# Performance work log

Measured on AMD Instinct MI355X. Metric: run time of the kernel, lower is better.

Reference implementation:

```python
import jax, jax.numpy as jnp
import numpy as np

EPS = 1e-5
SCALE = 2
K_UP = 5


def _conv(x, w, pad):
    return jax.lax.conv_general_dilated(
        x, w, window_strides=(1, 1), padding=[(pad, pad), (pad, pad)],
        dimension_numbers=("NCHW", "OIHW", "NCHW"))


def _bn(x, gamma, beta, mean, var):
    scale = gamma / jnp.sqrt(var + EPS)
    return x * scale[None, :, None, None] + (beta - mean * scale)[None, :, None, None]


def _pixel_shuffle(x, r):
    b, cr2, h, w = x.shape
    c = cr2 // (r * r)
    x = x.reshape(b, c, r, r, h, w)
    x = x.transpose(0, 1, 4, 2, 5, 3)  # b, c, h, r, w, r
    return x.reshape(b, c, h * r, w * r)


def setup_inputs() -> dict:
    key = jax.random.key(0)
    ks = jax.random.split(key, 6)
    c, c_mid, k_enc = 256, 64, 3
    n_k = (SCALE * K_UP) ** 2  # 100
    return {
        "x": jax.random.normal(ks[0], (2, c, 64, 64), jnp.float32),
        "comp_w": jax.random.normal(ks[1], (c_mid, c, 1, 1), jnp.float32) * 0.05,
        "comp_gamma": jnp.ones((c_mid,), jnp.float32),
        "comp_beta": jnp.zeros((c_mid,), jnp.float32),
        "comp_mean": jax.random.normal(ks[2], (c_mid,), jnp.float32) * 0.1,
        "comp_var": jax.random.uniform(ks[3], (c_mid,), jnp.float32, 0.5, 1.5),
        "enc_w": jax.random.normal(ks[4], (n_k, c_mid, k_enc, k_enc), jnp.float32) * 0.05,
        "enc_gamma": jnp.ones((n_k,), jnp.float32),
        "enc_beta": jnp.zeros((n_k,), jnp.float32),
        "enc_mean": jax.random.normal(ks[5], (n_k,), jnp.float32) * 0.1,
        "enc_var": jnp.ones((n_k,), jnp.float32),
    }


def reference(x, comp_w, comp_gamma, comp_beta, comp_mean, comp_var,
              enc_w, enc_gamma, enc_beta, enc_mean, enc_var):
    b, c, h, w = x.shape
    h_, w_ = h * SCALE, w * SCALE
    # comp: 1x1 conv -> BN -> ReLU
    W = jax.nn.relu(_bn(_conv(x, comp_w, 0), comp_gamma, comp_beta, comp_mean, comp_var))
    # enc: 3x3 conv -> BN (no relu)
    W = _bn(_conv(W, enc_w, 1), enc_gamma, enc_beta, enc_mean, enc_var)
    # pixel shuffle to [b, k_up^2, h_, w_] then softmax over kernel dim
    W = _pixel_shuffle(W, SCALE)
    W = jax.nn.softmax(W, axis=1)
    # nearest upsample x2
    Xu = jnp.repeat(jnp.repeat(x, SCALE, axis=2), SCALE, axis=3)
    # unfold: kernel k_up, dilation=SCALE, padding=k_up//2*SCALE
    pad = (K_UP // 2) * SCALE
    Xp = jnp.pad(Xu, ((0, 0), (0, 0), (pad, pad), (pad, pad)))
    patches = jnp.stack(
        [Xp[:, :, i * SCALE:i * SCALE + h_, j * SCALE:j * SCALE + w_]
         for i in range(K_UP) for j in range(K_UP)], axis=2)  # [b,c,k^2,h_,w_]
    return jnp.einsum("bkhw,bckhw->bchw", W, patches)
```

## Files before the change

kernel.cpp:

```cpp
#include <hip/hip_runtime.h>
#include <hip/hip_bf16.h>

typedef __hip_bfloat16 bf16;
#define EPSF 1e-5f

__global__ void k1_comp(const float* __restrict__ x, const float* __restrict__ w,
                        const float* __restrict__ gamma, const float* __restrict__ beta,
                        const float* __restrict__ mean, const float* __restrict__ var,
                        float* __restrict__ comp) {
    __shared__ float shx[2][32 * 64];
    const int pxt = blockIdx.x;
    const int ocg = blockIdx.y;
    const int b   = blockIdx.z;
    const int tid  = threadIdx.x;
    const int wave = tid >> 6, lane = tid & 63;
    const int oc0 = ocg * 32 + wave * 8;
    const int px0 = pxt << 6;
    const float* xb = x + b * (256 * 4096) + px0;

    float acc[8] = {0.f, 0.f, 0.f, 0.f, 0.f, 0.f, 0.f, 0.f};

    #pragma unroll
    for (int i = 0; i < 2; ++i) {
        int f4  = tid * 2 + i;
        int row = f4 >> 4, col4 = f4 & 15;
        float4 v = *(const float4*)(xb + row * 4096 + col4 * 4);
        *(float4*)(&shx[0][row * 64 + col4 * 4]) = v;
    }
    __syncthreads();

    for (int icc = 0; icc < 8; ++icc) {
        const int buf = icc & 1;
        if (icc < 7) {
            #pragma unroll
            for (int i = 0; i < 2; ++i) {
                int f4  = tid * 2 + i;
                int row = f4 >> 4, col4 = f4 & 15;
                float4 v = *(const float4*)(xb + ((icc + 1) * 32 + row) * 4096 + col4 * 4);
                *(float4*)(&shx[buf ^ 1][row * 64 + col4 * 4]) = v;
            }
        }
        #pragma unroll 8
        for (int ic_l = 0; ic_l < 32; ++ic_l) {
            float xv = shx[buf][ic_l * 64 + lane];
            const float* wp = w + icc * 32 + ic_l;
            #pragma unroll
            for (int m = 0; m < 8; ++m)
                acc[m] += xv * wp[(oc0 + m) * 256];
        }
        __syncthreads();
    }
    #pragma unroll
    for (int m = 0; m < 8; ++m) {
        int mo = oc0 + m;
        float s = gamma[mo] * rsqrtf(var[mo] + EPSF);
        float r = acc[m] * s + (beta[mo] - mean[mo] * s);
        comp[(b * 64 + mo) * 4096 + px0 + lane] = fmaxf(r, 0.f);
    }
}

__global__ void k2_enc_part(const float* __restrict__ comp, const float* __restrict__ w,
                            float* __restrict__ encp) {
    __shared__ float sh[8 * 630];
    const int tile = blockIdx.x;
    const int og   = blockIdx.y >> 2;
    const int icc  = blockIdx.y & 3;
    const int b    = blockIdx.z;
    const int ty0 = (tile >> 1) << 4;
    const int tx0 = (tile & 1) << 5;
    const int tid = threadIdx.x;
    const int tx = tid & 15, ty = tid >> 4;
    const int o0 = og * 5;

    float accA[5], accB[5];
    #pragma unroll
    for (int i = 0; i < 5; ++i) { accA[i] = 0.f; accB[i] = 0.f; }

    for (int ics = 0; ics < 2; ++ics) {
        if (ics) __syncthreads();
        const float* cb = comp + (b * 64 + icc * 16 + ics * 8) * 4096;
        for (int idx = tid; idx < 8 * 612; idx += 256) {
            int ic_l = idx / 612;
            int rem  = idx - ic_l * 612;
            int r = rem / 34;
            int c = rem - r * 34;
            int gy = ty0 + r - 1;
            int gx = tx0 + c - 1;
            float v = 0.f;
            if (gy >= 0 && gy < 64 && gx >= 0 && gx < 64)
                v = cb[(ic_l << 12) + (gy << 6) + gx];
            sh[ic_l * 630 + r * 35 + c] = v;
        }
        __syncthreads();

        #pragma unroll 2
        for (int ic_l = 0; ic_l < 8; ++ic_l) {
            const float* base = sh + ic_l * 630 + ty * 35 + 2 * tx;
            float t[3][4];
            #pragma unroll
            for (int dy = 0; dy < 3; ++dy)
                #pragma unroll
                for (int dx = 0; dx < 4; ++dx)
                    t[dy][dx] = base[dy * 35 + dx];
            const int ic = icc * 16 + ics * 8 + ic_l;
            #pragma unroll
            for (int o_l = 0; o_l < 5; ++o_l) {
                const float* wp = w + ((o0 + o_l) * 64 + ic) * 9;
                #pragma unroll
                for (int dy = 0; dy < 3; ++dy)
                    #pragma unroll
                    for (int dx = 0; dx < 3; ++dx) {
                        float wv = wp[dy * 3 + dx];
                        accA[o_l] += wv * t[dy][dx];
                        accB[o_l] += wv * t[dy][dx + 1];
                    }
            }
        }
    }
    const int pix = ((ty0 + ty) << 6) + tx0 + 2 * tx;
    #pragma unroll
    for (int o_l = 0; o_l < 5; ++o_l) {
        float2 v = {accA[o_l], accB[o_l]};
        *(float2*)(&encp[((icc * 2 + b) * 100 + o0 + o_l) * 4096 + pix]) = v;
    }
}

__global__ void k3_softmax(const float* __restrict__ encp,
                           const float* __restrict__ gamma, const float* __restrict__ beta,
                           const float* __restrict__ mean, const float* __restrict__ var,
                           bf16* __restrict__ Wsm) {
    int t = blockIdx.x * 64 + threadIdx.x;
    int pos = t & 4095;
    int g   = (t >> 12) & 3;
    int b   = t >> 14;
    float v[25];
    float mx = -1e30f;
    #pragma unroll
    for (int k = 0; k < 25; ++k) {
        int o = k * 4 + g;
        float a = 0.f;
        #pragma unroll
        for (int icc = 0; icc < 4; ++icc)
            a += encp[((icc * 2 + b) * 100 + o) * 4096 + pos];
        float s = gamma[o] * rsqrtf(var[o] + EPSF);
        v[k] = a * s + (beta[o] - mean[o] * s);
        mx = fmaxf(mx, v[k]);
    }
    float s = 0.f;
    #pragma unroll
    for (int k = 0; k < 25; ++k) { v[k] = __expf(v[k] - mx); s += v[k]; }
    float inv = 1.f / s;
    bf16* o = Wsm + ((b * 4 + g) * 25) * 4096 + pos;
    #pragma unroll
    for (int k = 0; k < 25; ++k) o[k * 4096] = __float2bfloat16(v[k] * inv);
}

__global__ void k4_gather(const float* __restrict__ x, const bf16* __restrict__ Wsm,
                          float* __restrict__ out) {
    __shared__ float4 patch[12 * 21];
    const int tile   = blockIdx.x;
    const int cchunk = blockIdx.y;
    const int b      = blockIdx.z;
    const int ly0 = (tile >> 2) << 3;
    const int lx0 = (tile & 3) << 4;
    const int tid = threadIdx.x;
    const int ph = tid >> 7;
    const int r  = tid & 127;
    const int ly = r >> 4, lx = r & 15;
    const int yl = ly0 + ly, xl = lx0 + lx;

    float w0[25], w1[25];
    {
        const bf16* wp0 = Wsm + ((b * 4 + ph * 2    ) * 25) * 4096 + yl * 64 + xl;
        const bf16* wp1 = Wsm + ((b * 4 + ph * 2 + 1) * 25) * 4096 + yl * 64 + xl;
        #pragma unroll
        for (int k = 0; k < 25; ++k) {
            w0[k] = __bfloat162float(wp0[k * 4096]);
            w1[k] = __bfloat162float(wp1[k * 4096]);
        }
    }
    const int pr = tid / 20, pc = tid % 20;
    const int gy = ly0 - 2 + pr, gx = lx0 - 2 + pc;
    const bool inb = (tid < 240) && (gy >= 0) && (gy < 64) && (gx >= 0) && (gx < 64);

    for (int cg = 0; cg < 4; ++cg) {
        const int c0 = cchunk * 16 + cg * 4;
        if (tid < 240) {
            float4 v = {0.f, 0.f, 0.f, 0.f};
            if (inb) {
                const float* xp = x + ((b * 256 + c0) * 4096) + gy * 64 + gx;
                v.x = xp[0]; v.y = xp[4096]; v.z = xp[8192]; v.w = xp[12288];
            }
            patch[pr * 21 + pc] = v;
        }
        __syncthreads();
        float4 a0 = {0.f, 0.f, 0.f, 0.f};
        float4 a1 = {0.f, 0.f, 0.f, 0.f};
        #pragma unroll
        for (int i = 0; i < 5; ++i) {
            #pragma unroll
            for (int j = 0; j < 5; ++j) {
                float4 xv = patch[(ly + i) * 21 + (lx + j)];
                float wa = w0[i * 5 + j], wb = w1[i * 5 + j];
                a0.x += wa * xv.x; a0.y += wa * xv.y; a0.z += wa * xv.z; a0.w += wa * xv.w;
                a1.x += wb * xv.x; a1.y += wb * xv.y; a1.z += wb * xv.z; a1.w += wb * xv.w;
            }
        }
        float* ob = out + (b * 256 + c0) * 16384 + (2 * yl + ph) * 128 + 2 * xl;
        float2 s0 = {a0.x, a1.x}; *(float2*)(ob)           = s0;
        float2 s1 = {a0.y, a1.y}; *(float2*)(ob + 16384)   = s1;
        float2 s2 = {a0.z, a1.z}; *(float2*)(ob + 32768)   = s2;
        float2 s3 = {a0.w, a1.w}; *(float2*)(ob + 49152)   = s3;
        __syncthreads();
    }
}

extern "C" void kernel_launch(void* const* d_in, const int* in_sizes, int n_in,
                              void* d_out, int out_size, void* d_ws, size_t ws_size,
                              hipStream_t stream) {
    const float* x          = (const float*)d_in[0];
    const float* comp_w     = (const float*)d_in[1];
    const float* comp_gamma = (const float*)d_in[2];
    const float* comp_beta  = (const float*)d_in[3];
    const float* comp_mean  = (const float*)d_in[4];
    const float* comp_var   = (const float*)d_in[5];
    const float* enc_w      = (const float*)d_in[6];
    const float* enc_gamma  = (const float*)d_in[7];
    const float* enc_beta   = (const float*)d_in[8];
    const float* enc_mean   = (const float*)d_in[9];
    const float* enc_var    = (const float*)d_in[10];
    float* out = (float*)d_out;

    float* ws   = (float*)d_ws;
    float* comp = ws;
    float* encp = ws + 524288;
    bf16*  Wsm  = (bf16*)(ws + 524288 + 3276800);

    k1_comp<<<dim3(64, 2, 2), dim3(256), 0, stream>>>(x, comp_w, comp_gamma, comp_beta,
                                                      comp_mean, comp_var, comp);
    k2_enc_part<<<dim3(8, 80, 2), dim3(256), 0, stream>>>(comp, enc_w, encp);
    k3_softmax<<<dim3(512), dim3(64), 0, stream>>>(encp, enc_gamma, enc_beta,
                                                   enc_mean, enc_var, Wsm);
    k4_gather<<<dim3(32, 16, 2), dim3(256), 0, stream>>>(x, Wsm, out);
}
```

Baseline: 154.9 us.

## Repack softmax weights pixel-major, split softmax across lanes, double-buffer gather patches

The softmax kernel now gives each pixel to four lanes, each handling eight of the 25 kernel taps, and combines the max and sum with cross-lane shuffles. It writes the bf16 weights in a pixel-major layout padded to 32 taps, so the gather kernel reads each pixel's weights as four 16-byte vector loads instead of 25 strided scalar loads. The gather kernel also double-buffers its shared-memory patch so the next channel group's global loads overlap with the current FMAs, removing one barrier per iteration. The costs are padded workspace traffic for the weights and more threads in the softmax launch.

New measurement: 196.5 us. 1.27x slower.

```diff
diff --git a/kernel.cpp b/kernel.cpp
--- a/kernel.cpp
+++ b/kernel.cpp
@@ -2,6 +2,7 @@
 #include <hip/hip_bf16.h>
 
 typedef __hip_bfloat16 bf16;
+typedef __attribute__((ext_vector_type(8))) unsigned short ushort8;
 #define EPSF 1e-5f
 
 __global__ void k1_comp(const float* __restrict__ x, const float* __restrict__ w,
@@ -129,35 +130,56 @@
                            const float* __restrict__ gamma, const float* __restrict__ beta,
                            const float* __restrict__ mean, const float* __restrict__ var,
                            bf16* __restrict__ Wsm) {
-    int t = blockIdx.x * 64 + threadIdx.x;
-    int pos = t & 4095;
-    int g   = (t >> 12) & 3;
-    int b   = t >> 14;
-    float v[25];
+    const int tid  = threadIdx.x;
+    const int lane = tid & 63, wave = tid >> 6;
+    const int il = lane & 15;
+    const int j  = lane >> 4;
+    const int item = blockIdx.x * 64 + wave * 16 + il;
+    const int pos = item & 4095;
+    const int g   = (item >> 12) & 3;
+    const int b   = item >> 14;
+    const size_t ICS = (size_t)200 * 4096;
+
+    float v[8];
     float mx = -1e30f;
     #pragma unroll
-    for (int k = 0; k < 25; ++k) {
-        int o = k * 4 + g;
+    for (int q = 0; q < 8; ++q) {
+        const int k = j * 8 + q;
         float a = 0.f;
-        #pragma unroll
-        for (int icc = 0; icc < 4; ++icc)
-            a += encp[((icc * 2 + b) * 100 + o) * 4096 + pos];
-        float s = gamma[o] * rsqrtf(var[o] + EPSF);
-        v[k] = a * s + (beta[o] - mean[o] * s);
-        mx = fmaxf(mx, v[k]);
-    }
-    float s = 0.f;
-    #pragma unroll
-    for (int k = 0; k < 25; ++k) { v[k] = __expf(v[k] - mx); s += v[k]; }
-    float inv = 1.f / s;
-    bf16* o = Wsm + ((b * 4 + g) * 25) * 4096 + pos;
-    #pragma unroll
-    for (int k = 0; k < 25; ++k) o[k * 4096] = __float2bfloat16(v[k] * inv);
+        if (k < 25) {
+            const int o = k * 4 + g;
+            const float* ep = encp + ((size_t)b * 100 + o) * 4096 + pos;
+            a = ((ep[0] + ep[ICS]) + ep[2 * ICS]) + ep[3 * ICS];
+            float s = gamma[o] * rsqrtf(var[o] + EPSF);
+            a = a * s + (beta[o] - mean[o] * s);
+            mx = fmaxf(mx, a);
+        }
+        v[q] = a;
+    }
+    mx = fmaxf(mx, __shfl_xor(mx, 16));
+    mx = fmaxf(mx, __shfl_xor(mx, 32));
+    float sum = 0.f;
+    #pragma unroll
+    for (int q = 0; q < 8; ++q) {
+        const int k = j * 8 + q;
+        float e = (k < 25) ? __expf(v[q] - mx) : 0.f;
+        v[q] = e;
+        sum += e;
+    }
+    sum += __shfl_xor(sum, 16);
+    sum += __shfl_xor(sum, 32);
+    const float inv = 1.f / sum;
+
+    ushort8 pk;
+    #pragma unroll
+    for (int q = 0; q < 8; ++q)
+        pk[q] = __bfloat16_as_ushort(__float2bfloat16(v[q] * inv));
+    *(ushort8*)(Wsm + (((size_t)(b * 4 + g) * 4096 + pos) * 32 + j * 8)) = pk;
 }
 
 __global__ void k4_gather(const float* __restrict__ x, const bf16* __restrict__ Wsm,
                           float* __restrict__ out) {
-    __shared__ float4 patch[12 * 21];
+    __shared__ float4 patch[2][12 * 21];
     const int tile   = blockIdx.x;
     const int cchunk = blockIdx.y;
     const int b      = blockIdx.z;
@@ -171,47 +193,61 @@
 
     float w0[25], w1[25];
     {
-        const bf16* wp0 = Wsm + ((b * 4 + ph * 2    ) * 25) * 4096 + yl * 64 + xl;
-        const bf16* wp1 = Wsm + ((b * 4 + ph * 2 + 1) * 25) * 4096 + yl * 64 + xl;
+        const ushort8* p0 = (const ushort8*)(Wsm +
+            ((size_t)(b * 4 + ph * 2) * 4096 + (yl * 64 + xl)) * 32);
+        const ushort8* p1 = p0 + 16384;
+        ushort8 q0[4] = {p0[0], p0[1], p0[2], p0[3]};
+        ushort8 q1[4] = {p1[0], p1[1], p1[2], p1[3]};
         #pragma unroll
         for (int k = 0; k < 25; ++k) {
-            w0[k] = __bfloat162float(wp0[k * 4096]);
-            w1[k] = __bfloat162float(wp1[k * 4096]);
+            w0[k] = __uint_as_float(((unsigned)q0[k >> 3][k & 7]) << 16);
+            w1[k] = __uint_as_float(((unsigned)q1[k >> 3][k & 7]) << 16);
         }
     }
     const int pr = tid / 20, pc = tid % 20;
     const int gy = ly0 - 2 + pr, gx = lx0 - 2 + pc;
-    const bool inb = (tid < 240) && (gy >= 0) && (gy < 64) && (gx >= 0) && (gx < 64);
-
+    const bool act = (tid < 240);
+    const bool inb = act && (gy >= 0) && (gy < 64) && (gx >= 0) && (gx < 64);
+
+    {
+        float4 v = {0.f, 0.f, 0.f, 0.f};
+        if (inb) {
+            const float* xp = x + ((b * 256 + cchunk * 16) * 4096) + gy * 64 + gx;
+            v.x = xp[0]; v.y = xp[4096]; v.z = xp[8192]; v.w = xp[12288];
+        }
+        if (act) patch[0][pr * 21 + pc] = v;
+    }
+    __syncthreads();
+
+    #pragma unroll
     for (int cg = 0; cg < 4; ++cg) {
-        const int c0 = cchunk * 16 + cg * 4;
-        if (tid < 240) {
-            float4 v = {0.f, 0.f, 0.f, 0.f};
-            if (inb) {
-                const float* xp = x + ((b * 256 + c0) * 4096) + gy * 64 + gx;
-                v.x = xp[0]; v.y = xp[4096]; v.z = xp[8192]; v.w = xp[12288];
-            }
-            patch[pr * 21 + pc] = v;
-        }
-        __syncthreads();
+        float4 nv = {0.f, 0.f, 0.f, 0.f};
+        if (cg < 3 && inb) {
+            const float* xp = x + ((b * 256 + cchunk * 16 + (cg + 1) * 4) * 4096) + gy * 64 + gx;
+            nv.x = xp[0]; nv.y = xp[4096]; nv.z = xp[8192]; nv.w = xp[12288];
+        }
         float4 a0 = {0.f, 0.f, 0.f, 0.f};
         float4 a1 = {0.f, 0.f, 0.f, 0.f};
+        const float4* pp = patch[cg & 1];
         #pragma unroll
         for (int i = 0; i < 5; ++i) {
             #pragma unroll
-            for (int j = 0; j < 5; ++j) {
-                float4 xv = patch[(ly + i) * 21 + (lx + j)];
-                float wa = w0[i * 5 + j], wb = w1[i * 5 + j];
+            for (int jx = 0; jx < 5; ++jx) {
+                float4 xv = pp[(ly + i) * 21 + (lx + jx)];
+                float wa = w0[i * 5 + jx], wb = w1[i * 5 + jx];
                 a0.x += wa * xv.x; a0.y += wa * xv.y; a0.z += wa * xv.z; a0.w += wa * xv.w;
                 a1.x += wb * xv.x; a1.y += wb * xv.y; a1.z += wb * xv.z; a1.w += wb * xv.w;
             }
         }
-        float* ob = out + (b * 256 + c0) * 16384 + (2 * yl + ph) * 128 + 2 * xl;
+        if (cg < 3 && act) patch[(cg + 1) & 1][pr * 21 + pc] = nv;
+
+        const int c0 = cchunk * 16 + cg * 4;
+        float* ob = out + (size_t)(b * 256 + c0) * 16384 + (2 * yl + ph) * 128 + 2 * xl;
         float2 s0 = {a0.x, a1.x}; *(float2*)(ob)           = s0;
         float2 s1 = {a0.y, a1.y}; *(float2*)(ob + 16384)   = s1;
         float2 s2 = {a0.z, a1.z}; *(float2*)(ob + 32768)   = s2;
         float2 s3 = {a0.w, a1.w}; *(float2*)(ob + 49152)   = s3;
-        __syncthreads();
+        if (cg < 3) __syncthreads();
     }
 }
 
@@ -239,7 +275,7 @@
     k1_comp<<<dim3(64, 2, 2), dim3(256), 0, stream>>>(x, comp_w, comp_gamma, comp_beta,
                                                       comp_mean, comp_var, comp);
     k2_enc_part<<<dim3(8, 80, 2), dim3(256), 0, stream>>>(comp, enc_w, encp);
-    k3_softmax<<<dim3(512), dim3(64), 0, stream>>>(encp, enc_gamma, enc_beta,
-                                                   enc_mean, enc_var, Wsm);
+    k3_softmax<<<dim3(512), dim3(256), 0, stream>>>(encp, enc_gamma, enc_beta,
+                                                    enc_mean, enc_var, Wsm);
     k4_gather<<<dim3(32, 16, 2), dim3(256), 0, stream>>>(x, Wsm, out);
 }
```

## Split softmax kernel across four waves and halve per-wave channels in comp

Applied to the files above, without the earlier changes.

The softmax kernel now uses 256 threads per block, with each of four waves handling a slice of the 25 kernel taps. The max and sum are combined across waves through shared memory. The 1x1 compression kernel now computes 4 output channels per wave instead of 8 and launches twice as many blocks. Both changes aim to raise parallelism and occupancy in small, latency-bound kernels, at the cost of re-reading x tiles from global memory more often and adding block-level syncs.

Measured after the change: 147.0 us. 1.05x faster.

```diff
diff --git a/kernel.cpp b/kernel.cpp
--- a/kernel.cpp
+++ b/kernel.cpp
@@ -14,11 +14,11 @@
     const int b   = blockIdx.z;
     const int tid  = threadIdx.x;
     const int wave = tid >> 6, lane = tid & 63;
-    const int oc0 = ocg * 32 + wave * 8;
+    const int oc0 = ocg * 16 + wave * 4;
     const int px0 = pxt << 6;
     const float* xb = x + b * (256 * 4096) + px0;
 
-    float acc[8] = {0.f, 0.f, 0.f, 0.f, 0.f, 0.f, 0.f, 0.f};
+    float acc[4] = {0.f, 0.f, 0.f, 0.f};
 
     #pragma unroll
     for (int i = 0; i < 2; ++i) {
@@ -45,13 +45,13 @@
             float xv = shx[buf][ic_l * 64 + lane];
             const float* wp = w + icc * 32 + ic_l;
             #pragma unroll
-            for (int m = 0; m < 8; ++m)
+            for (int m = 0; m < 4; ++m)
                 acc[m] += xv * wp[(oc0 + m) * 256];
         }
         __syncthreads();
     }
     #pragma unroll
-    for (int m = 0; m < 8; ++m) {
+    for (int m = 0; m < 4; ++m) {
         int mo = oc0 + m;
         float s = gamma[mo] * rsqrtf(var[mo] + EPSF);
         float r = acc[m] * s + (beta[mo] - mean[mo] * s);
@@ -129,30 +129,48 @@
                            const float* __restrict__ gamma, const float* __restrict__ beta,
                            const float* __restrict__ mean, const float* __restrict__ var,
                            bf16* __restrict__ Wsm) {
-    int t = blockIdx.x * 64 + threadIdx.x;
-    int pos = t & 4095;
-    int g   = (t >> 12) & 3;
-    int b   = t >> 14;
-    float v[25];
+    __shared__ float red[2][4][64];
+    const int tid  = threadIdx.x;
+    const int lane = tid & 63, wv = tid >> 6;
+    const int item = blockIdx.x * 64 + lane;
+    const int pos = item & 4095;
+    const int g   = (item >> 12) & 3;
+    const int b   = item >> 14;
+    const int kbase = (wv == 0) ? 0 : 1 + 6 * wv;
+    const int cnt   = (wv == 0) ? 7 : 6;
+    const size_t ICS = (size_t)200 * 4096;
+
+    float v[7];
     float mx = -1e30f;
     #pragma unroll
-    for (int k = 0; k < 25; ++k) {
-        int o = k * 4 + g;
-        float a = 0.f;
-        #pragma unroll
-        for (int icc = 0; icc < 4; ++icc)
-            a += encp[((icc * 2 + b) * 100 + o) * 4096 + pos];
-        float s = gamma[o] * rsqrtf(var[o] + EPSF);
-        v[k] = a * s + (beta[o] - mean[o] * s);
-        mx = fmaxf(mx, v[k]);
-    }
+    for (int q = 0; q < 7; ++q) {
+        if (q < cnt) {
+            const int o = (kbase + q) * 4 + g;
+            const float* ep = encp + ((size_t)b * 100 + o) * 4096 + pos;
+            float a = ((ep[0] + ep[ICS]) + ep[2 * ICS]) + ep[3 * ICS];
+            float s = gamma[o] * rsqrtf(var[o] + EPSF);
+            v[q] = a * s + (beta[o] - mean[o] * s);
+            mx = fmaxf(mx, v[q]);
+        }
+    }
+    red[0][wv][lane] = mx;
+    __syncthreads();
+    mx = fmaxf(fmaxf(red[0][0][lane], red[0][1][lane]),
+               fmaxf(red[0][2][lane], red[0][3][lane]));
     float s = 0.f;
     #pragma unroll
-    for (int k = 0; k < 25; ++k) { v[k] = __expf(v[k] - mx); s += v[k]; }
-    float inv = 1.f / s;
-    bf16* o = Wsm + ((b * 4 + g) * 25) * 4096 + pos;
-    #pragma unroll
-    for (int k = 0; k < 25; ++k) o[k * 4096] = __float2bfloat16(v[k] * inv);
+    for (int q = 0; q < 7; ++q) {
+        if (q < cnt) { v[q] = __expf(v[q] - mx); s += v[q]; }
+    }
+    red[1][wv][lane] = s;
+    __syncthreads();
+    s = ((red[1][0][lane] + red[1][1][lane]) + red[1][2][lane]) + red[1][3][lane];
+    const float inv = 1.f / s;
+    bf16* o_ = Wsm + ((size_t)(b * 4 + g) * 25 + kbase) * 4096 + pos;
+    #pragma unroll
+    for (int q = 0; q < 7; ++q) {
+        if (q < cnt) o_[q * 4096] = __float2bfloat16(v[q] * inv);
+    }
 }
 
 __global__ void k4_gather(const float* __restrict__ x, const bf16* __restrict__ Wsm,
@@ -236,10 +254,10 @@
     float* encp = ws + 524288;
     bf16*  Wsm  = (bf16*)(ws + 524288 + 3276800);
 
-    k1_comp<<<dim3(64, 2, 2), dim3(256), 0, stream>>>(x, comp_w, comp_gamma, comp_beta,
+    k1_comp<<<dim3(64, 4, 2), dim3(256), 0, stream>>>(x, comp_w, comp_gamma, comp_beta,
                                                       comp_mean, comp_var, comp);
     k2_enc_part<<<dim3(8, 80, 2), dim3(256), 0, stream>>>(comp, enc_w, encp);
-    k3_softmax<<<dim3(512), dim3(64), 0, stream>>>(encp, enc_gamma, enc_beta,
-                                                   enc_mean, enc_var, Wsm);
+    k3_softmax<<<dim3(512), dim3(256), 0, stream>>>(encp, enc_gamma, enc_beta,
+                                                    enc_mean, enc_var, Wsm);
     k4_gather<<<dim3(32, 16, 2), dim3(256), 0, stream>>>(x, Wsm, out);
 }
```
